# Kernel tuning notes

Hardware: AMD Instinct MI355X
Metric: run time of the kernel (lower is better)

## Reference

```python
import jax, jax.numpy as jnp
import numpy as np

K = 9            # connections per output pixel
GA = 2           # global additional samples
RA = 2           # relative additional samples
VS = 4 + GA + RA # 2^rank neighbours + sampled
REGION = 12      # int(0.25 * 48) per spatial dim
MMULT = 0.1
MIN_SIGMA = 0.05
SIGMA_SCALE = 0.05
SIGMA_BOOST = 2.0


def setup_inputs() -> dict:
    key = jax.random.key(0)
    ks = jax.random.split(key, 8)
    b, cin, h, w = 8, 128, 48, 48
    cout = 256
    hidden = cin * 4

    def lin_init(k, fan_out, fan_in):
        bound = 1.0 / np.sqrt(fan_in)
        kw, kb = jax.random.split(k)
        W = jax.random.uniform(kw, (fan_out, fan_in), minval=-bound, maxval=bound, dtype=jnp.float32)
        bb = jax.random.uniform(kb, (fan_out,), minval=-bound, maxval=bound, dtype=jnp.float32)
        return W, bb

    x = jax.random.normal(ks[0], (b, cin, h, w), dtype=jnp.float32)
    W1, b1 = lin_init(ks[1], hidden, 2)          # toparams layer 1 (adaptive=False -> 2 coord inputs)
    W2, b2 = lin_init(ks[2], 3 * K, hidden)      # toparams layer 2 -> k means (2d) + k sigmas
    Wu, bu = lin_init(ks[3], cout, K * cin)      # unify linear
    gints = jax.random.randint(ks[4], (b, h, w, K, GA, 2), 0, h, dtype=jnp.int32)      # global samples (h==w)
    roff = jax.random.randint(ks[5], (b, h, w, K, RA, 2), 0, REGION, dtype=jnp.int32)  # relative offsets
    return {"x": x, "W1": W1, "b1": b1, "W2": W2, "b2": b2, "Wu": Wu, "bu": bu,
            "gints": gints, "roff": roff}


def reference(x, W1, b1, W2, b2, Wu, bu, gints, roff):
    b, c, h, w = x.shape
    s = jnp.array([h, w], dtype=x.dtype)                       # spatial range per dim
    s_int = jnp.array([h, w], dtype=jnp.int32)

    # normalized coordinate grid in [0,1], (h, w, 2) with [.,.,0]=row, [.,.,1]=col
    rows = jnp.arange(h, dtype=x.dtype) / (h - 1)
    cols = jnp.arange(w, dtype=x.dtype) / (w - 1)
    coords = jnp.stack(jnp.meshgrid(rows, cols, indexing='ij'), axis=-1)

    # hypernetwork: per-pixel coords -> K 2d mean offsets + K sigmas
    inp = jnp.broadcast_to(coords, (b, h, w, 2))
    hid = jax.nn.relu(inp @ W1.T + b1)
    params = hid @ W2.T + b2                                   # (b,h,w,3K)
    means_raw = params[..., :2 * K].reshape(b, h, w, K, 2)
    sig_raw = params[..., 2 * K:]                              # (b,h,w,K)

    # mids: inverse of the sigmoid scaling applied to the pixel's own coordinate
    pix = coords * (s - 1)                                     # pixel coordinates
    sc = pix / (s - 1) * 0.9999 + 0.00005
    mids = jnp.log(sc / (1.0 - sc))                            # (h,w,2)

    # transform_means: sigmoid -> [0, s-1]
    means = jax.nn.sigmoid(mids[None, :, :, None, :] + MMULT * means_raw) * (s - 1)  # (b,h,w,K,2)
    # transform_sigmas: softplus(. + boost) + min, per-dim scale, then sigma_scale
    sigmas = (jax.nn.softplus(sig_raw + SIGMA_BOOST) + MIN_SIGMA)[..., None] * s * SIGMA_SCALE  # (b,h,w,K,2)

    # ---- integer index generation (non-differentiable) ----
    fl = jnp.floor(jax.lax.stop_gradient(means)).astype(jnp.int32)   # (b,h,w,K,2)
    combos = jnp.array([[0, 0], [0, 1], [1, 0], [1, 1]], dtype=jnp.int32)
    neigh = fl[..., None, :] + combos                                 # (b,h,w,K,4,2)
    rel = fl[..., None, :] + roff - REGION // 2                       # (b,h,w,K,RA,2)
    ints = jnp.concatenate([neigh, gints, rel], axis=-2) % s_int      # (b,h,w,K,VS,2)

    # duplicate masking: zero any tuple that occurred earlier along VS
    eq = jnp.all(ints[..., :, None, :] == ints[..., None, :, :], axis=-1)  # (...,VS,VS)
    lower = jnp.tril(jnp.ones((VS, VS), dtype=bool), k=-1)
    dups = jnp.any(eq & lower, axis=-1)                               # (b,h,w,K,VS)

    # unnormalized gaussian densities of integer points under (means, sigmas)
    diff = (ints.astype(x.dtype) - means[..., None, :]) / sigmas[..., None, :]
    props = jnp.exp(-0.5 * jnp.sum(diff * diff, axis=-1))             # (b,h,w,K,VS)
    props = jnp.where(dups, jnp.zeros((), x.dtype), props)
    weights = props / jnp.sum(props, axis=-1, keepdims=True)          # mvalues are all-ones

    # irregular gather of input channel vectors at sampled pixels
    lin = ints[..., 0] * w + ints[..., 1]                             # (b,h,w,K,VS)
    flat = x.transpose(0, 2, 3, 1).reshape(b, h * w, c)
    feats = flat[jnp.arange(b)[:, None], lin.reshape(b, -1)]          # (b, h*w*K*VS, c)
    feats = feats.reshape(b, h, w, K, VS, c)

    feats = jnp.einsum('bhwkvc,bhwkv->bhwkc', feats, weights)         # weighted reduce over VS
    feats = feats.reshape(b, h, w, K * c)
    out = feats @ Wu.T + bu                                           # unify linear
    return out.transpose(0, 3, 1, 2)                                  # (b, cout, h, w)
```

## Files before the change

### kernel.cpp

```cpp
#include <hip/hip_runtime.h>
#include <hip/hip_bf16.h>

#define BB 8
#define CIN 128
#define HH 48
#define WW 48
#define HW 2304
#define KK 9
#define COUT 256
#define KC 1152
#define MM 18432
#define MT 32
#define SFP 136

typedef short bf16x8_t __attribute__((ext_vector_type(8)));
typedef float f32x16_t __attribute__((ext_vector_type(16)));
typedef float f32x4_t  __attribute__((ext_vector_type(4)));

static __device__ __forceinline__ float b2f(short u) {
    union { unsigned int i; float f; } c;
    c.i = ((unsigned int)(unsigned short)u) << 16;
    return c.f;
}

__global__ __launch_bounds__(256) void prep_kernel(
    const float* __restrict__ x, __hip_bfloat16* __restrict__ xT,
    const float* __restrict__ Wu, bf16x8_t* __restrict__ Bp,
    const float* __restrict__ W1, const float* __restrict__ b1,
    const float* __restrict__ W2, const float* __restrict__ b2,
    float* __restrict__ means, float* __restrict__ sigmas, int* __restrict__ fls)
{
    int bid = blockIdx.x;
    int t = threadIdx.x;

    if (bid < 576) {
        __shared__ float tile[64][65];
        int ij0 = (bid % 36) * 64;
        int c0  = ((bid / 36) % 2) * 64;
        int b   = bid / 72;
        int ijl = t & 63, cl = t >> 6;
        #pragma unroll
        for (int i = 0; i < 16; i++) {
            int cc = i*4 + cl;
            tile[cc][ijl] = x[(size_t)(b*CIN + c0 + cc) * HW + ij0 + ijl];
        }
        __syncthreads();
        int cl2 = t & 63, ijl2 = t >> 6;
        #pragma unroll
        for (int i = 0; i < 16; i++) {
            int ij = i*4 + ijl2;
            xT[(size_t)(b*HW + ij0 + ij) * CIN + c0 + cl2] = __float2bfloat16(tile[cl2][ij]);
        }
    } else if (bid < 720) {
        int idx = (bid - 576) * 256 + t;
        int lane = idx & 63;
        int rest = idx >> 6;
        int s = rest % 72, g = rest / 72;
        int r = lane & 31, qq = lane >> 5;
        const float* src = Wu + (size_t)(g*32 + r) * KC + s*16 + qq*8;
        union { bf16x8_t v; __hip_bfloat16 h[8]; } o;
        #pragma unroll
        for (int j = 0; j < 8; j++) o.h[j] = __float2bfloat16(src[j]);
        Bp[idx] = o.v;
    } else {
        int wave = t >> 6, lane = t & 63;
        int p = (bid - 720) * 4 + wave;
        int iy = p / WW, ix = p % WW;
        float ryf = (float)iy / 47.0f;
        float rxf = (float)ix / 47.0f;
        double ry = (double)ryf, rx = (double)rxf;

        double h[8];
        #pragma unroll
        for (int jj = 0; jj < 8; jj++) {
            int j = lane*8 + jj;
            double v = ry * (double)W1[j*2+0] + rx * (double)W1[j*2+1] + (double)b1[j];
            h[jj] = v > 0.0 ? v : 0.0;
        }
        double par[27];
        #pragma unroll
        for (int o = 0; o < 27; o++) {
            const float4* w4 = (const float4*)(W2 + (size_t)o*512 + lane*8);
            float4 wa = w4[0], wb = w4[1];
            double s = (double)wa.x*h[0] + (double)wa.y*h[1]
                     + (double)wa.z*h[2] + (double)wa.w*h[3]
                     + (double)wb.x*h[4] + (double)wb.y*h[5]
                     + (double)wb.z*h[6] + (double)wb.w*h[7];
            par[o] = s;
        }
        #pragma unroll
        for (int o = 0; o < 27; o++) {
            #pragma unroll
            for (int d = 1; d < 64; d <<= 1)
                par[o] += __shfl_xor(par[o], d, 64);
            par[o] += (double)b2[o];
        }
        if (lane < KK) {
            int k = lane;
            double scy = ry * 0.9999 + 5e-05;
            double scx = rx * 0.9999 + 5e-05;
            double midy = log(scy / (1.0 - scy));
            double midx = log(scx / (1.0 - scx));
            double zy = midy + 0.1 * par[2*k+0];
            double zx = midx + 0.1 * par[2*k+1];
            double my = 47.0 / (1.0 + exp(-zy));
            double mx = 47.0 / (1.0 + exp(-zx));
            double sr = par[18 + k] + 2.0;
            double sp = (sr > 0.0 ? sr : 0.0) + log1p(exp(-fabs(sr)));
            double sg = (sp + 0.05) * 48.0 * 0.05;
            means[(p*KK + k)*2 + 0] = (float)my;
            means[(p*KK + k)*2 + 1] = (float)mx;
            sigmas[p*KK + k] = (float)sg;
            fls[(p*KK + k)*2 + 0] = (int)floor(my);
            fls[(p*KK + k)*2 + 1] = (int)floor(mx);
        }
    }
}

__global__ __launch_bounds__(512, 4) void fused_kernel(
    const float* __restrict__ means, const float* __restrict__ sigmas,
    const int* __restrict__ fls, const int* __restrict__ gints,
    const int* __restrict__ roff, const short* __restrict__ xT,
    const bf16x8_t* __restrict__ Bp, const float* __restrict__ bu,
    float* __restrict__ out)
{
    __shared__ int2 s_tap[KK*MT*8];
    __shared__ __align__(16) short s_feat[2][MT*SFP];

    int t = threadIdx.x;
    int m0 = blockIdx.x * MT;
    int b  = m0 / HW;
    int ij0 = m0 % HW;

    if (t < KK*MT) {
        int p = t;
        int k = p >> 5, row = p & 31;
        int ij = ij0 + row;
        int bij = m0 + row;
        int fy = fls[(ij*KK + k)*2 + 0];
        int fx = fls[(ij*KK + k)*2 + 1];
        float my = means[(ij*KK + k)*2 + 0];
        float mx = means[(ij*KK + k)*2 + 1];
        float sg = sigmas[ij*KK + k];
        int lins[8]; float ws[8];
        #pragma unroll
        for (int v = 0; v < 8; v++) {
            int iy, ix;
            if (v < 4) {
                iy = fy + (v >> 1); ix = fx + (v & 1);
            } else if (v < 6) {
                int base = ((bij*KK + k)*2 + (v - 4)) * 2;
                iy = gints[base]; ix = gints[base + 1];
            } else {
                int base = ((bij*KK + k)*2 + (v - 6)) * 2;
                iy = fy + roff[base] - 6; ix = fx + roff[base + 1] - 6;
            }
            iy = ((iy % HH) + HH) % HH;
            ix = ((ix % WW) + WW) % WW;
            lins[v] = iy * WW + ix;
            float dy = ((float)iy - my) / sg;
            float dx = ((float)ix - mx) / sg;
            ws[v] = expf(-0.5f * (dy*dy + dx*dx));
        }
        #pragma unroll
        for (int v = 1; v < 8; v++) {
            bool dup = false;
            #pragma unroll
            for (int u = 0; u < 8; u++) if (u < v) dup = dup || (lins[u] == lins[v]);
            if (dup) ws[v] = 0.0f;
        }
        float sum = 0.0f;
        #pragma unroll
        for (int v = 0; v < 8; v++) sum += ws[v];
        float inv = 1.0f / sum;
        #pragma unroll
        for (int v = 0; v < 8; v++)
            s_tap[p*8+v] = make_int2(lins[v], __float_as_int(ws[v] * inv));
    }
    __syncthreads();

    const short* xb = xT + (size_t)b * (HW * CIN);
    int lane = t & 63, wave = t >> 6;
    int r = lane & 31, q = lane >> 5;
    int grow = t >> 4, gc0 = (t & 15) << 3;

    f32x16_t acc = {};
    bf16x8_t Bf[8];
    bf16x8_t tapA[4], tapB[4];
    float    wgtA[4], wgtB[4];

    {
        int base = (wave*72 + 0)*64 + lane;
        #pragma unroll
        for (int si = 0; si < 8; si++) Bf[si] = Bp[base + si*64];
        const int2* tp = &s_tap[(0*MT + grow)*8];
        #pragma unroll
        for (int v = 0; v < 4; v++) {
            int2 e = tp[v];
            wgtA[v] = __int_as_float(e.y);
            tapA[v] = *(const bf16x8_t*)(xb + (size_t)e.x * CIN + gc0);
        }
    }

    for (int k = 0; k < KK; k++) {
        const int2* tp = &s_tap[(k*MT + grow)*8];
        #pragma unroll
        for (int v = 0; v < 4; v++) {
            int2 e = tp[4+v];
            wgtB[v] = __int_as_float(e.y);
            tapB[v] = *(const bf16x8_t*)(xb + (size_t)e.x * CIN + gc0);
        }
        float a0[8];
        #pragma unroll
        for (int j = 0; j < 8; j++) a0[j] = 0.0f;
        #pragma unroll
        for (int v = 0; v < 4; v++) {
            float w = wgtA[v]; bf16x8_t d8 = tapA[v];
            #pragma unroll
            for (int j = 0; j < 8; j++) a0[j] += w * b2f(d8[j]);
        }
        if (k + 1 < KK) {
            const int2* tn = &s_tap[((k+1)*MT + grow)*8];
            #pragma unroll
            for (int v = 0; v < 4; v++) {
                int2 e = tn[v];
                wgtA[v] = __int_as_float(e.y);
                tapA[v] = *(const bf16x8_t*)(xb + (size_t)e.x * CIN + gc0);
            }
        }
        #pragma unroll
        for (int v = 0; v < 4; v++) {
            float w = wgtB[v]; bf16x8_t d8 = tapB[v];
            #pragma unroll
            for (int j = 0; j < 8; j++) a0[j] += w * b2f(d8[j]);
        }
        union { bf16x8_t v8; __hip_bfloat16 hh[8]; } o;
        #pragma unroll
        for (int j = 0; j < 8; j++) o.hh[j] = __float2bfloat16(a0[j]);
        *(bf16x8_t*)(&s_feat[k & 1][grow*SFP + gc0]) = o.v8;
        __syncthreads();
        const short* fb = s_feat[k & 1];
        #pragma unroll
        for (int si = 0; si < 8; si++) {
            bf16x8_t a = *(const bf16x8_t*)(fb + r*SFP + si*16 + q*8);
            acc = __builtin_amdgcn_mfma_f32_32x32x16_bf16(a, Bf[si], acc, 0, 0, 0);
        }
        if (k + 1 < KK) {
            int base = (wave*72 + (k+1)*8)*64 + lane;
            #pragma unroll
            for (int si = 0; si < 8; si++) Bf[si] = Bp[base + si*64];
        }
    }

    int n = wave*32 + r;
    float bv = bu[n];
    float* oc = out + ((size_t)b * COUT + n) * HW + ij0;
    #pragma unroll
    for (int g4 = 0; g4 < 4; g4++) {
        f32x4_t vv;
        vv[0] = acc[g4*4+0] + bv;
        vv[1] = acc[g4*4+1] + bv;
        vv[2] = acc[g4*4+2] + bv;
        vv[3] = acc[g4*4+3] + bv;
        *(f32x4_t*)(oc + g4*8 + q*4) = vv;
    }
}

extern "C" void kernel_launch(void* const* d_in, const int* in_sizes, int n_in,
                              void* d_out, int out_size, void* d_ws, size_t ws_size,
                              hipStream_t stream)
{
    const float* x   = (const float*)d_in[0];
    const float* W1  = (const float*)d_in[1];
    const float* b1  = (const float*)d_in[2];
    const float* W2  = (const float*)d_in[3];
    const float* b2  = (const float*)d_in[4];
    const float* Wu  = (const float*)d_in[5];
    const float* bu  = (const float*)d_in[6];
    const int* gints = (const int*)d_in[7];
    const int* roff  = (const int*)d_in[8];
    float* out = (float*)d_out;

    char* ws = (char*)d_ws;
    float* ws_means  = (float*)(ws + 0);
    float* ws_sigma  = (float*)(ws + 165888);
    int*   ws_fl     = (int*  )(ws + 248832);
    short* ws_xT     = (short*)(ws + 414720);
    bf16x8_t* ws_bp  = (bf16x8_t*)(ws + 5133312);

    prep_kernel<<<1296, 256, 0, stream>>>(x, (__hip_bfloat16*)ws_xT, Wu, ws_bp,
                                          W1, b1, W2, b2,
                                          ws_means, ws_sigma, ws_fl);
    fused_kernel<<<MM/MT, 512, 0, stream>>>(ws_means, ws_sigma, ws_fl, gints, roff,
                                            ws_xT, ws_bp, bu, out);
}
```

Baseline: 149.7 us.

## Prefetch all eight taps of next k and use lightweight LDS barrier

The gather pipeline now prefetches all eight tap vectors for the next connection k before reducing the current one, replacing the half-and-half A/B split, and fully unrolls the k loop. __syncthreads is replaced with an inline-asm barrier that waits only on LDS counters, so outstanding global loads stay in flight across the barrier. Tap indices are pre-multiplied by CIN in shared memory to save a multiply per load. The deeper prefetch raises register pressure (16 bf16x8 tap registers plus the B fragments), which may lower occupancy.

```diff
diff --git a/kernel.cpp b/kernel.cpp
--- a/kernel.cpp
+++ b/kernel.cpp
@@ -12,6 +12,8 @@
 #define MM 18432
 #define MT 32
 #define SFP 136
+
+#define LIGHT_BARRIER() asm volatile("s_waitcnt lgkmcnt(0)\n\ts_barrier" ::: "memory")
 
 typedef short bf16x8_t __attribute__((ext_vector_type(8)));
 typedef float f32x16_t __attribute__((ext_vector_type(16)));
@@ -175,9 +177,9 @@
         float inv = 1.0f / sum;
         #pragma unroll
         for (int v = 0; v < 8; v++)
-            s_tap[p*8+v] = make_int2(lins[v], __float_as_int(ws[v] * inv));
-    }
-    __syncthreads();
+            s_tap[p*8+v] = make_int2(lins[v] * CIN, __float_as_int(ws[v] * inv));
+    }
+    LIGHT_BARRIER();
 
     const short* xb = xT + (size_t)b * (HW * CIN);
     int lane = t & 63, wave = t >> 6;
@@ -186,69 +188,65 @@
 
     f32x16_t acc = {};
     bf16x8_t Bf[8];
-    bf16x8_t tapA[4], tapB[4];
-    float    wgtA[4], wgtB[4];
+    bf16x8_t tapC[8];
+    float    wgtC[8];
 
     {
+        const int2* tp = &s_tap[(0*MT + grow)*8];
+        #pragma unroll
+        for (int v = 0; v < 8; v++) {
+            int2 e = tp[v];
+            wgtC[v] = __int_as_float(e.y);
+            tapC[v] = *(const bf16x8_t*)(xb + e.x + gc0);
+        }
         int base = (wave*72 + 0)*64 + lane;
         #pragma unroll
         for (int si = 0; si < 8; si++) Bf[si] = Bp[base + si*64];
-        const int2* tp = &s_tap[(0*MT + grow)*8];
-        #pragma unroll
-        for (int v = 0; v < 4; v++) {
-            int2 e = tp[v];
-            wgtA[v] = __int_as_float(e.y);
-            tapA[v] = *(const bf16x8_t*)(xb + (size_t)e.x * CIN + gc0);
-        }
-    }
-
+    }
+
+    #pragma unroll
     for (int k = 0; k < KK; k++) {
-        const int2* tp = &s_tap[(k*MT + grow)*8];
-        #pragma unroll
-        for (int v = 0; v < 4; v++) {
-            int2 e = tp[4+v];
-            wgtB[v] = __int_as_float(e.y);
-            tapB[v] = *(const bf16x8_t*)(xb + (size_t)e.x * CIN + gc0);
-        }
-        float a0[8];
-        #pragma unroll
-        for (int j = 0; j < 8; j++) a0[j] = 0.0f;
-        #pragma unroll
-        for (int v = 0; v < 4; v++) {
-            float w = wgtA[v]; bf16x8_t d8 = tapA[v];
-            #pragma unroll
-            for (int j = 0; j < 8; j++) a0[j] += w * b2f(d8[j]);
-        }
+        bf16x8_t tapN[8];
+        float    wgtN[8];
         if (k + 1 < KK) {
             const int2* tn = &s_tap[((k+1)*MT + grow)*8];
             #pragma unroll
-            for (int v = 0; v < 4; v++) {
+            for (int v = 0; v < 8; v++) {
                 int2 e = tn[v];
-                wgtA[v] = __int_as_float(e.y);
-                tapA[v] = *(const bf16x8_t*)(xb + (size_t)e.x * CIN + gc0);
-            }
-        }
-        #pragma unroll
-        for (int v = 0; v < 4; v++) {
-            float w = wgtB[v]; bf16x8_t d8 = tapB[v];
-            #pragma unroll
-            for (int j = 0; j < 8; j++) a0[j] += w * b2f(d8[j]);
-        }
-        union { bf16x8_t v8; __hip_bfloat16 hh[8]; } o;
-        #pragma unroll
-        for (int j = 0; j < 8; j++) o.hh[j] = __float2bfloat16(a0[j]);
-        *(bf16x8_t*)(&s_feat[k & 1][grow*SFP + gc0]) = o.v8;
-        __syncthreads();
-        const short* fb = s_feat[k & 1];
-        #pragma unroll
-        for (int si = 0; si < 8; si++) {
-            bf16x8_t a = *(const bf16x8_t*)(fb + r*SFP + si*16 + q*8);
-            acc = __builtin_amdgcn_mfma_f32_32x32x16_bf16(a, Bf[si], acc, 0, 0, 0);
+                wgtN[v] = __int_as_float(e.y);
+                tapN[v] = *(const bf16x8_t*)(xb + e.x + gc0);
+            }
+        }
+        {
+            float a0[8];
+            #pragma unroll
+            for (int j = 0; j < 8; j++) a0[j] = 0.0f;
+            #pragma unroll
+            for (int v = 0; v < 8; v++) {
+                float w = wgtC[v]; bf16x8_t d8 = tapC[v];
+                #pragma unroll
+                for (int j = 0; j < 8; j++) a0[j] += w * b2f(d8[j]);
+            }
+            union { bf16x8_t v8; __hip_bfloat16 hh[8]; } o;
+            #pragma unroll
+            for (int j = 0; j < 8; j++) o.hh[j] = __float2bfloat16(a0[j]);
+            *(bf16x8_t*)(&s_feat[k & 1][grow*SFP + gc0]) = o.v8;
+        }
+        LIGHT_BARRIER();
+        {
+            const short* fb = s_feat[k & 1];
+            #pragma unroll
+            for (int si = 0; si < 8; si++) {
+                bf16x8_t a = *(const bf16x8_t*)(fb + r*SFP + si*16 + q*8);
+                acc = __builtin_amdgcn_mfma_f32_32x32x16_bf16(a, Bf[si], acc, 0, 0, 0);
+            }
         }
         if (k + 1 < KK) {
             int base = (wave*72 + (k+1)*8)*64 + lane;
             #pragma unroll
             for (int si = 0; si < 8; si++) Bf[si] = Bp[base + si*64];
+            #pragma unroll
+            for (int v = 0; v < 8; v++) { tapC[v] = tapN[v]; wgtC[v] = wgtN[v]; }
         }
     }
 
```

Result: no change. 147.9 us (-1.2%).
